# Optimization experiments

Measured on AMD Instinct MI355X. Metric: run time of the kernel, lower is better.

Reference implementation:

```python
import jax, jax.numpy as jnp
import numpy as np

NUM_HEADS = 16
THETA = 10000.0


def setup_inputs() -> dict:
    key = jax.random.key(0)
    ks = jax.random.split(key, 5)
    B, S, D = 2, 2048, 1024
    scale = 1.0 / np.sqrt(D)
    return {
        "x": jax.random.normal(ks[0], (B, S, D), dtype=jnp.float32),
        "Wq": jax.random.normal(ks[1], (D, D), dtype=jnp.float32) * scale,
        "Wk": jax.random.normal(ks[2], (D, D), dtype=jnp.float32) * scale,
        "Wv": jax.random.normal(ks[3], (D, D), dtype=jnp.float32) * scale,
        "Wo": jax.random.normal(ks[4], (D, D), dtype=jnp.float32) * scale,
    }


def _rope(t, cos, sin):
    # t: [B, H, S, d_k], interleaved pair rotation.
    t1 = t[..., 0::2]
    t2 = t[..., 1::2]
    r1 = t1 * cos - t2 * sin
    r2 = t1 * sin + t2 * cos
    # re-interleave
    out = jnp.stack([r1, r2], axis=-1)
    return out.reshape(t.shape)


def reference(x, Wq, Wk, Wv, Wo):
    B, S, D = x.shape
    H = NUM_HEADS
    dk = D // H

    # projections (Linear: y = x @ W^T)
    Q = jnp.einsum("bsd,ed->bse", x, Wq).reshape(B, S, H, dk).transpose(0, 2, 1, 3)
    K = jnp.einsum("bsd,ed->bse", x, Wk).reshape(B, S, H, dk).transpose(0, 2, 1, 3)
    V = jnp.einsum("bsd,ed->bse", x, Wv).reshape(B, S, H, dk).transpose(0, 2, 1, 3)

    # RoPE angles: [S, dk/2]
    inv_freq = THETA ** (-jnp.arange(0, dk, 2, dtype=jnp.float32) / dk)
    ang = jnp.arange(S, dtype=jnp.float32)[:, None] * inv_freq[None, :]
    cos, sin = jnp.cos(ang), jnp.sin(ang)  # broadcast over [B, H, S, dk/2]
    Q = _rope(Q, cos, sin)
    K = _rope(K, cos, sin)

    # causal SDPA
    scores = jnp.einsum("bhqd,bhkd->bhqk", Q, K) / jnp.sqrt(jnp.float32(dk))
    causal = jnp.tril(jnp.ones((S, S), dtype=bool))
    scores = jnp.where(causal, scores, jnp.finfo(scores.dtype).min)
    attn = jax.nn.softmax(scores, axis=-1)
    out = jnp.einsum("bhqk,bhkd->bhqd", attn, V)

    out = out.transpose(0, 2, 1, 3).reshape(B, S, D)
    return jnp.einsum("bsd,ed->bse", out, Wo)
```

## Files before the change

### kernel.cpp

```cpp
#include <hip/hip_runtime.h>
#include <hip/hip_bf16.h>

#define B_   2
#define S_   2048
#define H_   16
#define DK_  64
#define D_   1024
#define BS_  4096
#define N3_  3072

typedef __attribute__((ext_vector_type(8))) short short8;
typedef __attribute__((ext_vector_type(4))) float floatx4;
typedef __hip_bfloat16 bf16;

__device__ inline void load_lds16(const bf16* g, bf16* l) {
    __builtin_amdgcn_global_load_lds(
        (const __attribute__((address_space(1))) void*)g,
        (__attribute__((address_space(3))) void*)l, 16, 0, 0);
}

__device__ inline unsigned int pack2bf16(float a, float b) {
    __hip_bfloat162 h = __float22bfloat162_rn(make_float2(a, b));
    return *(unsigned int*)&h;
}

__global__ void cvt_all(const float* __restrict__ x,  const float* __restrict__ wq,
                        const float* __restrict__ wk, const float* __restrict__ wv,
                        const float* __restrict__ wo,
                        bf16* __restrict__ xb, bf16* __restrict__ wcat, bf16* __restrict__ wob) {
    const int blk = blockIdx.x;
    const float* src; bf16* dst; int base;
    if (blk < 4096)      { src = x;  dst = xb;             base = blk * 1024; }
    else if (blk < 5120) { src = wq; dst = wcat;           base = (blk - 4096) * 1024; }
    else if (blk < 6144) { src = wk; dst = wcat + 1048576; base = (blk - 5120) * 1024; }
    else if (blk < 7168) { src = wv; dst = wcat + 2097152; base = (blk - 6144) * 1024; }
    else                 { src = wo; dst = wob;            base = (blk - 7168) * 1024; }
    const int i = base + threadIdx.x * 4;
    float4 v = *(const float4*)(src + i);
    *(uint2*)(dst + i) = make_uint2(pack2bf16(v.x, v.y), pack2bf16(v.z, v.w));
}

__global__ __launch_bounds__(256)
void gemm_qkv(const bf16* __restrict__ A, const bf16* __restrict__ Bw,
              bf16* __restrict__ Cqk, bf16* __restrict__ Vt) {
    __shared__ __align__(16) bf16 lA[128 * 32];
    __shared__ __align__(16) bf16 lB[128 * 32];
    const int t = threadIdx.x;
    const int lane = t & 63, w = t >> 6;
    const int quad = lane >> 4, l16 = lane & 15;
    const int m0 = blockIdx.x * 128, n0 = blockIdx.y * 128;
    const int wm = (w & 1) * 64, wn = (w >> 1) * 64;

    floatx4 acc[4][4];
#pragma unroll
    for (int i = 0; i < 4; i++)
#pragma unroll
        for (int j = 0; j < 4; j++) acc[i][j] = (floatx4){0.f, 0.f, 0.f, 0.f};

    const int srow = t >> 2;
    const int scol = (t & 3) * 8;
    const bf16* pA0 = A + (size_t)(m0 + srow) * D_ + scol;
    const bf16* pA1 = A + (size_t)(m0 + 64 + srow) * D_ + scol;
    const bf16* pB0 = Bw + (size_t)(n0 + srow) * D_ + scol;
    const bf16* pB1 = Bw + (size_t)(n0 + 64 + srow) * D_ + scol;

    for (int kt = 0; kt < D_; kt += 32) {
        load_lds16(pA0, lA + t * 8);
        load_lds16(pA1, lA + 2048 + t * 8);
        load_lds16(pB0, lB + t * 8);
        load_lds16(pB1, lB + 2048 + t * 8);
        pA0 += 32; pA1 += 32; pB0 += 32; pB1 += 32;
        __syncthreads();

        short8 af[4], bfr[4];
#pragma unroll
        for (int i = 0; i < 4; i++)
            af[i] = *(const short8*)&lA[(wm + i * 16 + l16) * 32 + quad * 8];
#pragma unroll
        for (int j = 0; j < 4; j++)
            bfr[j] = *(const short8*)&lB[(wn + j * 16 + l16) * 32 + quad * 8];
#pragma unroll
        for (int i = 0; i < 4; i++)
#pragma unroll
            for (int j = 0; j < 4; j++)
                acc[i][j] = __builtin_amdgcn_mfma_f32_16x16x32_bf16(af[i], bfr[j], acc[i][j], 0, 0, 0);
        __syncthreads();
    }

    if (n0 < 2 * D_) {
#pragma unroll
        for (int i = 0; i < 4; i++) {
            const int row = m0 + wm + i * 16 + quad * 4;
#pragma unroll
            for (int j = 0; j < 4; j++) {
                const int col = n0 + wn + j * 16 + l16;
#pragma unroll
                for (int r = 0; r < 4; r++)
                    Cqk[(size_t)(row + r) * N3_ + col] = __float2bfloat16(acc[i][j][r]);
            }
        }
    } else {
#pragma unroll
        for (int i = 0; i < 4; i++) {
            const int row0 = m0 + wm + i * 16 + quad * 4;
            const int bb = row0 >> 11;
            const int ss = row0 & 2047;
#pragma unroll
            for (int j = 0; j < 4; j++) {
                const int c = n0 + wn + j * 16 + l16 - 2 * D_;
                const int h = c >> 6, d = c & 63;
                *(uint2*)(Vt + (((size_t)bb * H_ + h) * 64 + d) * S_ + ss) =
                    make_uint2(pack2bf16(acc[i][j][0], acc[i][j][1]),
                               pack2bf16(acc[i][j][2], acc[i][j][3]));
            }
        }
    }
}

__global__ void rope_kernel(const bf16* __restrict__ QKV,
                            bf16* __restrict__ Qr, bf16* __restrict__ Kr) {
    int tid = blockIdx.x * blockDim.x + threadIdx.x;
    if (tid >= B_ * S_ * H_ * 32) return;
    const int i = tid & 31;
    const int h = (tid >> 5) & (H_ - 1);
    const int bs = tid >> 9;
    const int s = bs & (S_ - 1);
    const int b = bs >> 11;

    const bf16* base = QKV + (size_t)bs * N3_ + h * 64 + 2 * i;
    const float q0 = __bfloat162float(base[0]);
    const float q1 = __bfloat162float(base[1]);
    const float k0 = __bfloat162float(base[D_]);
    const float k1 = __bfloat162float(base[D_ + 1]);

    const float freq = exp2f(-(float)(2 * i) * 0.2076205059304601f);
    const float ang = (float)s * freq;
    float sn, cs;
    sincosf(ang, &sn, &cs);

    const float QS = 0.18033688011112042f;
    const size_t off = ((size_t)(b * H_ + h) * S_ + s) * 64 + 2 * i;
    *(unsigned int*)(Qr + off) = pack2bf16((q0 * cs - q1 * sn) * QS, (q0 * sn + q1 * cs) * QS);
    *(unsigned int*)(Kr + off) = pack2bf16(k0 * cs - k1 * sn, k0 * sn + k1 * cs);
}

__global__ __launch_bounds__(256)
void attn_kernel(const bf16* __restrict__ Qr, const bf16* __restrict__ Kr,
                 const bf16* __restrict__ Vt, bf16* __restrict__ Ob) {
    __shared__ __align__(16) bf16 lK0[64 * 64], lK1[64 * 64];
    __shared__ __align__(16) bf16 lV0[64 * 64], lV1[64 * 64];
    __shared__ __align__(16) bf16 lP[4][16][36];

    const int t = threadIdx.x;
    const int w = t >> 6, lane = t & 63;
    const int quad = lane >> 4, l16 = lane & 15;
    const int bh = blockIdx.y;
    const int b = bh >> 4, h = bh & 15;
    const int qblk = 31 - (int)blockIdx.x;
    const int q0w = qblk * 64 + w * 16;
    const int q = q0w + l16;

    const bf16* Qb = Qr + (size_t)bh * S_ * 64;
    const bf16* Kb = Kr + (size_t)bh * S_ * 64;
    const bf16* Vb = Vt + (size_t)bh * 64 * S_;

    const int srow = t >> 3;
    const int sj   = (t & 7) ^ (srow & 7);
    const int swz = l16 & 7;
    const int pA = quad ^ swz;
    const int pB = (4 + quad) ^ swz;

    const bf16* qrow = Qb + (size_t)q * 64;
    short8 bq[2];
    bq[0] = *(const short8*)(qrow + quad * 8);
    bq[1] = *(const short8*)(qrow + 32 + quad * 8);

    float lacc = 0.f;
    floatx4 o[4];
#pragma unroll
    for (int ct = 0; ct < 4; ct++) o[ct] = (floatx4){0.f, 0.f, 0.f, 0.f};

    auto stage = [&](bf16* dK, bf16* dV, int kb) {
        const bf16* gK = Kb + (size_t)(kb + srow) * 64 + sj * 8;
        const bf16* gV = Vb + (size_t)srow * S_ + kb + sj * 8;
        load_lds16(gK,                   dK + t * 8);
        load_lds16(gK + 32 * 64,         dK + 2048 + t * 8);
        load_lds16(gV,                   dV + t * 8);
        load_lds16(gV + (size_t)32 * S_, dV + 2048 + t * 8);
    };

    auto computeStep = [&](const bf16* lKc, const bf16* lVc, int kb, bool need_mask) {
#pragma unroll
        for (int c = 0; c < 2; c++) {
            floatx4 s[2];
#pragma unroll
            for (int k2 = 0; k2 < 2; k2++) {
                const int kt = c * 2 + k2;
                const short8 k0 = *(const short8*)&lKc[(kt * 16 + l16) * 64 + pA * 8];
                const short8 k1 = *(const short8*)&lKc[(kt * 16 + l16) * 64 + pB * 8];
                floatx4 z = (floatx4){0.f, 0.f, 0.f, 0.f};
                z = __builtin_amdgcn_mfma_f32_16x16x32_bf16(k0, bq[0], z, 0, 0, 0);
                z = __builtin_amdgcn_mfma_f32_16x16x32_bf16(k1, bq[1], z, 0, 0, 0);
                s[k2] = z;
            }
            float rs = 0.f;
#pragma unroll
            for (int k2 = 0; k2 < 2; k2++) {
                float p[4];
#pragma unroll
                for (int r = 0; r < 4; r++) {
                    float v = s[k2][r];
                    if (need_mask) {
                        const int key = kb + (c * 2 + k2) * 16 + quad * 4 + r;
                        if (key > q) v = -1e30f;
                    }
                    p[r] = __builtin_amdgcn_exp2f(v);
                    rs += p[r];
                }
                *(uint2*)&lP[w][l16][k2 * 16 + quad * 4] =
                    make_uint2(pack2bf16(p[0], p[1]), pack2bf16(p[2], p[3]));
            }
            lacc += rs;
            const int pc = c ? pB : pA;
            const short8 bp = *(const short8*)&lP[w][l16][quad * 8];
#pragma unroll
            for (int ct = 0; ct < 4; ct++) {
                const short8 av = *(const short8*)&lVc[(ct * 16 + l16) * 64 + pc * 8];
                o[ct] = __builtin_amdgcn_mfma_f32_16x16x32_bf16(av, bp, o[ct], 0, 0, 0);
            }
        }
    };

    const int nsteps = qblk + 1;
    stage(lK0, lV0, 0);
    __syncthreads();
    for (int st = 0; st < nsteps; ++st) {
        const bool even = (st & 1) == 0;
        const bf16* cK = even ? lK0 : lK1;  const bf16* cV = even ? lV0 : lV1;
        bf16* nK = even ? lK1 : lK0;        bf16* nV = even ? lV1 : lV0;
        if (st + 1 < nsteps) stage(nK, nV, (st + 1) * 64);
        computeStep(cK, cV, st * 64, st == nsteps - 1);
        __syncthreads();
    }

    float l = lacc;
    l += __shfl_xor(l, 16);
    l += __shfl_xor(l, 32);
    const float invl = 1.0f / l;
    bf16* orow = Ob + ((size_t)(b * S_ + q) * H_ + h) * 64;
#pragma unroll
    for (int ct = 0; ct < 4; ct++)
        *(uint2*)(orow + ct * 16 + quad * 4) =
            make_uint2(pack2bf16(o[ct][0] * invl, o[ct][1] * invl),
                       pack2bf16(o[ct][2] * invl, o[ct][3] * invl));
}

__global__ __launch_bounds__(256)
void gemm_out(const bf16* __restrict__ A, const bf16* __restrict__ Bw,
              float* __restrict__ C) {
    __shared__ __align__(16) bf16 lA[128 * 32];
    __shared__ __align__(16) bf16 lB[64 * 32];
    const int t = threadIdx.x;
    const int lane = t & 63, w = t >> 6;
    const int quad = lane >> 4, l16 = lane & 15;
    const int m0 = blockIdx.x * 128, n0 = blockIdx.y * 64;
    const int wm = (w & 1) * 64, wn = (w >> 1) * 32;

    floatx4 acc[4][2];
#pragma unroll
    for (int i = 0; i < 4; i++)
#pragma unroll
        for (int j = 0; j < 2; j++) acc[i][j] = (floatx4){0.f, 0.f, 0.f, 0.f};

    const int srow = t >> 2;
    const int scol = (t & 3) * 8;
    const bf16* pA0 = A + (size_t)(m0 + srow) * D_ + scol;
    const bf16* pA1 = A + (size_t)(m0 + 64 + srow) * D_ + scol;
    const bf16* pB0 = Bw + (size_t)(n0 + srow) * D_ + scol;

    for (int kt = 0; kt < D_; kt += 32) {
        load_lds16(pA0, lA + t * 8);
        load_lds16(pA1, lA + 2048 + t * 8);
        load_lds16(pB0, lB + t * 8);
        pA0 += 32; pA1 += 32; pB0 += 32;
        __syncthreads();

        short8 af[4], bfr[2];
#pragma unroll
        for (int i = 0; i < 4; i++)
            af[i] = *(const short8*)&lA[(wm + i * 16 + l16) * 32 + quad * 8];
#pragma unroll
        for (int j = 0; j < 2; j++)
            bfr[j] = *(const short8*)&lB[(wn + j * 16 + l16) * 32 + quad * 8];
#pragma unroll
        for (int i = 0; i < 4; i++)
#pragma unroll
            for (int j = 0; j < 2; j++)
                acc[i][j] = __builtin_amdgcn_mfma_f32_16x16x32_bf16(af[i], bfr[j], acc[i][j], 0, 0, 0);
        __syncthreads();
    }

#pragma unroll
    for (int i = 0; i < 4; i++) {
        const int row = m0 + wm + i * 16 + quad * 4;
#pragma unroll
        for (int j = 0; j < 2; j++) {
            const int col = n0 + wn + j * 16 + l16;
#pragma unroll
            for (int r = 0; r < 4; r++)
                C[(size_t)(row + r) * D_ + col] = acc[i][j][r];
        }
    }
}

extern "C" void kernel_launch(void* const* d_in, const int* in_sizes, int n_in,
                              void* d_out, int out_size, void* d_ws, size_t ws_size,
                              hipStream_t stream) {
    const float* x  = (const float*)d_in[0];
    const float* Wq = (const float*)d_in[1];
    const float* Wk = (const float*)d_in[2];
    const float* Wv = (const float*)d_in[3];
    const float* Wo = (const float*)d_in[4];
    float* out = (float*)d_out;

    char* ws = (char*)d_ws;
    bf16* xb   = (bf16*)(ws);
    bf16* Wcat = (bf16*)(ws + 8388608);
    bf16* Wob  = (bf16*)(ws + 14680064);
    bf16* QKVb = (bf16*)(ws + 16777216);
    bf16* Qr   = (bf16*)(ws + 41943040);
    bf16* Kr   = (bf16*)(ws + 50331648);
    bf16* Vt   = (bf16*)(ws + 58720256);
    bf16* Ob   = QKVb;

    cvt_all<<<8192, 256, 0, stream>>>(x, Wq, Wk, Wv, Wo, xb, Wcat, Wob);
    gemm_qkv<<<dim3(32, 24), 256, 0, stream>>>(xb, Wcat, QKVb, Vt);
    rope_kernel<<<8192, 256, 0, stream>>>(QKVb, Qr, Kr);
    attn_kernel<<<dim3(32, B_ * H_), 256, 0, stream>>>(Qr, Kr, Vt, Ob);
    gemm_out<<<dim3(32, 16), 256, 0, stream>>>(Ob, Wob, out);
}
```

Measured before the change: 203.7 us.

## Use 32x32 MFMA in attention and K=64 swizzled LDS tiles in GEMMs

The attention kernel drops to 128 threads, with two waves of 32 query rows each. Both QK^T and PV now use the 32x32x16 bf16 MFMA, with a swizzled K/V LDS layout and a reshaped P staging buffer. Both GEMMs double the K tile to 64 per iteration and XOR-swizzle the LDS layout, which halves the barrier count and should avoid bank conflicts. The costs are more registers in attention, fewer waves per block, and larger LDS use in the GEMMs.

```diff
diff --git a/kernel.cpp b/kernel.cpp
--- a/kernel.cpp
+++ b/kernel.cpp
@@ -11,6 +11,7 @@
 
 typedef __attribute__((ext_vector_type(8))) short short8;
 typedef __attribute__((ext_vector_type(4))) float floatx4;
+typedef __attribute__((ext_vector_type(16))) float floatx16;
 typedef __hip_bfloat16 bf16;
 
 __device__ inline void load_lds16(const bf16* g, bf16* l) {
@@ -43,8 +44,8 @@
 __global__ __launch_bounds__(256)
 void gemm_qkv(const bf16* __restrict__ A, const bf16* __restrict__ Bw,
               bf16* __restrict__ Cqk, bf16* __restrict__ Vt) {
-    __shared__ __align__(16) bf16 lA[128 * 32];
-    __shared__ __align__(16) bf16 lB[128 * 32];
+    __shared__ __align__(16) bf16 lA[128 * 64];
+    __shared__ __align__(16) bf16 lB[128 * 64];
     const int t = threadIdx.x;
     const int lane = t & 63, w = t >> 6;
     const int quad = lane >> 4, l16 = lane & 15;
@@ -57,33 +58,39 @@
 #pragma unroll
         for (int j = 0; j < 4; j++) acc[i][j] = (floatx4){0.f, 0.f, 0.f, 0.f};
 
-    const int srow = t >> 2;
-    const int scol = (t & 3) * 8;
-    const bf16* pA0 = A + (size_t)(m0 + srow) * D_ + scol;
-    const bf16* pA1 = A + (size_t)(m0 + 64 + srow) * D_ + scol;
-    const bf16* pB0 = Bw + (size_t)(n0 + srow) * D_ + scol;
-    const bf16* pB1 = Bw + (size_t)(n0 + 64 + srow) * D_ + scol;
-
-    for (int kt = 0; kt < D_; kt += 32) {
-        load_lds16(pA0, lA + t * 8);
-        load_lds16(pA1, lA + 2048 + t * 8);
-        load_lds16(pB0, lB + t * 8);
-        load_lds16(pB1, lB + 2048 + t * 8);
-        pA0 += 32; pA1 += 32; pB0 += 32; pB1 += 32;
-        __syncthreads();
-
-        short8 af[4], bfr[4];
-#pragma unroll
-        for (int i = 0; i < 4; i++)
-            af[i] = *(const short8*)&lA[(wm + i * 16 + l16) * 32 + quad * 8];
-#pragma unroll
-        for (int j = 0; j < 4; j++)
-            bfr[j] = *(const short8*)&lB[(wn + j * 16 + l16) * 32 + quad * 8];
-#pragma unroll
-        for (int i = 0; i < 4; i++)
-#pragma unroll
-            for (int j = 0; j < 4; j++)
-                acc[i][j] = __builtin_amdgcn_mfma_f32_16x16x32_bf16(af[i], bfr[j], acc[i][j], 0, 0, 0);
+    const int srow = t >> 3;
+    const int sj   = (t & 7) ^ (srow & 7);
+
+    for (int kt = 0; kt < D_; kt += 64) {
+#pragma unroll
+        for (int r = 0; r < 4; r++)
+            load_lds16(A + (size_t)(m0 + r * 32 + srow) * D_ + kt + sj * 8,
+                       lA + r * 2048 + t * 8);
+#pragma unroll
+        for (int r = 0; r < 4; r++)
+            load_lds16(Bw + (size_t)(n0 + r * 32 + srow) * D_ + kt + sj * 8,
+                       lB + r * 2048 + t * 8);
+        __syncthreads();
+
+#pragma unroll
+        for (int kh = 0; kh < 2; kh++) {
+            short8 af[4], bfr[4];
+#pragma unroll
+            for (int i = 0; i < 4; i++) {
+                const int row = wm + i * 16 + l16;
+                af[i] = *(const short8*)&lA[row * 64 + ((kh * 4 + quad) ^ (row & 7)) * 8];
+            }
+#pragma unroll
+            for (int j = 0; j < 4; j++) {
+                const int row = wn + j * 16 + l16;
+                bfr[j] = *(const short8*)&lB[row * 64 + ((kh * 4 + quad) ^ (row & 7)) * 8];
+            }
+#pragma unroll
+            for (int i = 0; i < 4; i++)
+#pragma unroll
+                for (int j = 0; j < 4; j++)
+                    acc[i][j] = __builtin_amdgcn_mfma_f32_16x16x32_bf16(af[i], bfr[j], acc[i][j], 0, 0, 0);
+        }
         __syncthreads();
     }
 
@@ -144,21 +151,20 @@
     *(unsigned int*)(Kr + off) = pack2bf16(k0 * cs - k1 * sn, k0 * sn + k1 * cs);
 }
 
-__global__ __launch_bounds__(256)
+__global__ __launch_bounds__(128)
 void attn_kernel(const bf16* __restrict__ Qr, const bf16* __restrict__ Kr,
                  const bf16* __restrict__ Vt, bf16* __restrict__ Ob) {
     __shared__ __align__(16) bf16 lK0[64 * 64], lK1[64 * 64];
     __shared__ __align__(16) bf16 lV0[64 * 64], lV1[64 * 64];
-    __shared__ __align__(16) bf16 lP[4][16][36];
+    __shared__ __align__(16) bf16 lP[2][32][34];
 
     const int t = threadIdx.x;
     const int w = t >> 6, lane = t & 63;
-    const int quad = lane >> 4, l16 = lane & 15;
+    const int l32 = lane & 31, hi = lane >> 5;
     const int bh = blockIdx.y;
     const int b = bh >> 4, h = bh & 15;
     const int qblk = 31 - (int)blockIdx.x;
-    const int q0w = qblk * 64 + w * 16;
-    const int q = q0w + l16;
+    const int q = qblk * 64 + w * 32 + l32;
 
     const bf16* Qb = Qr + (size_t)bh * S_ * 64;
     const bf16* Kb = Kr + (size_t)bh * S_ * 64;
@@ -166,67 +172,72 @@
 
     const int srow = t >> 3;
     const int sj   = (t & 7) ^ (srow & 7);
-    const int swz = l16 & 7;
-    const int pA = quad ^ swz;
-    const int pB = (4 + quad) ^ swz;
-
-    const bf16* qrow = Qb + (size_t)q * 64;
-    short8 bq[2];
-    bq[0] = *(const short8*)(qrow + quad * 8);
-    bq[1] = *(const short8*)(qrow + 32 + quad * 8);
+
+    short8 bq[4];
+    {
+        const bf16* qrow = Qb + (size_t)q * 64;
+#pragma unroll
+        for (int ks = 0; ks < 4; ks++)
+            bq[ks] = *(const short8*)(qrow + ks * 16 + hi * 8);
+    }
 
     float lacc = 0.f;
-    floatx4 o[4];
-#pragma unroll
-    for (int ct = 0; ct < 4; ct++) o[ct] = (floatx4){0.f, 0.f, 0.f, 0.f};
+    floatx16 o[2];
+#pragma unroll
+    for (int dt = 0; dt < 2; dt++)
+#pragma unroll
+        for (int r = 0; r < 16; r++) o[dt][r] = 0.f;
 
     auto stage = [&](bf16* dK, bf16* dV, int kb) {
-        const bf16* gK = Kb + (size_t)(kb + srow) * 64 + sj * 8;
-        const bf16* gV = Vb + (size_t)srow * S_ + kb + sj * 8;
-        load_lds16(gK,                   dK + t * 8);
-        load_lds16(gK + 32 * 64,         dK + 2048 + t * 8);
-        load_lds16(gV,                   dV + t * 8);
-        load_lds16(gV + (size_t)32 * S_, dV + 2048 + t * 8);
+#pragma unroll
+        for (int r = 0; r < 4; r++)
+            load_lds16(Kb + (size_t)(kb + r * 16 + srow) * 64 + sj * 8,
+                       dK + r * 1024 + t * 8);
+#pragma unroll
+        for (int r = 0; r < 4; r++)
+            load_lds16(Vb + (size_t)(r * 16 + srow) * S_ + kb + sj * 8,
+                       dV + r * 1024 + t * 8);
     };
 
     auto computeStep = [&](const bf16* lKc, const bf16* lVc, int kb, bool need_mask) {
 #pragma unroll
-        for (int c = 0; c < 2; c++) {
-            floatx4 s[2];
-#pragma unroll
-            for (int k2 = 0; k2 < 2; k2++) {
-                const int kt = c * 2 + k2;
-                const short8 k0 = *(const short8*)&lKc[(kt * 16 + l16) * 64 + pA * 8];
-                const short8 k1 = *(const short8*)&lKc[(kt * 16 + l16) * 64 + pB * 8];
-                floatx4 z = (floatx4){0.f, 0.f, 0.f, 0.f};
-                z = __builtin_amdgcn_mfma_f32_16x16x32_bf16(k0, bq[0], z, 0, 0, 0);
-                z = __builtin_amdgcn_mfma_f32_16x16x32_bf16(k1, bq[1], z, 0, 0, 0);
-                s[k2] = z;
-            }
-            float rs = 0.f;
-#pragma unroll
-            for (int k2 = 0; k2 < 2; k2++) {
-                float p[4];
-#pragma unroll
-                for (int r = 0; r < 4; r++) {
-                    float v = s[k2][r];
-                    if (need_mask) {
-                        const int key = kb + (c * 2 + k2) * 16 + quad * 4 + r;
-                        if (key > q) v = -1e30f;
-                    }
-                    p[r] = __builtin_amdgcn_exp2f(v);
-                    rs += p[r];
+        for (int kt = 0; kt < 2; kt++) {
+            floatx16 z;
+#pragma unroll
+            for (int r = 0; r < 16; r++) z[r] = 0.f;
+            const int krow = kt * 32 + l32;
+#pragma unroll
+            for (int ks = 0; ks < 4; ks++) {
+                const short8 ak = *(const short8*)
+                    &lKc[krow * 64 + (((ks * 2 + hi) ^ (krow & 7)) * 8)];
+                z = __builtin_amdgcn_mfma_f32_32x32x16_bf16(ak, bq[ks], z, 0, 0, 0);
+            }
+            float p[16];
+#pragma unroll
+            for (int r = 0; r < 16; r++) {
+                float v = z[r];
+                if (need_mask) {
+                    const int key = kb + kt * 32 + (r & 3) + 8 * (r >> 2) + 4 * hi;
+                    if (key > q) v = -1e30f;
                 }
-                *(uint2*)&lP[w][l16][k2 * 16 + quad * 4] =
-                    make_uint2(pack2bf16(p[0], p[1]), pack2bf16(p[2], p[3]));
-            }
-            lacc += rs;
-            const int pc = c ? pB : pA;
-            const short8 bp = *(const short8*)&lP[w][l16][quad * 8];
-#pragma unroll
-            for (int ct = 0; ct < 4; ct++) {
-                const short8 av = *(const short8*)&lVc[(ct * 16 + l16) * 64 + pc * 8];
-                o[ct] = __builtin_amdgcn_mfma_f32_16x16x32_bf16(av, bp, o[ct], 0, 0, 0);
+                p[r] = __builtin_amdgcn_exp2f(v);
+                lacc += p[r];
+            }
+#pragma unroll
+            for (int rq = 0; rq < 4; rq++)
+                *(uint2*)&lP[w][l32][8 * rq + 4 * hi] =
+                    make_uint2(pack2bf16(p[rq * 4 + 0], p[rq * 4 + 1]),
+                               pack2bf16(p[rq * 4 + 2], p[rq * 4 + 3]));
+#pragma unroll
+            for (int kl = 0; kl < 2; kl++) {
+                const short8 bp = *(const short8*)&lP[w][l32][kl * 16 + hi * 8];
+#pragma unroll
+                for (int dt = 0; dt < 2; dt++) {
+                    const int vrow = dt * 32 + l32;
+                    const short8 av = *(const short8*)
+                        &lVc[vrow * 64 + (((kt * 4 + kl * 2 + hi) ^ (vrow & 7)) * 8)];
+                    o[dt] = __builtin_amdgcn_mfma_f32_32x32x16_bf16(av, bp, o[dt], 0, 0, 0);
+                }
             }
         }
     };
@@ -243,23 +254,25 @@
         __syncthreads();
     }
 
-    float l = lacc;
-    l += __shfl_xor(l, 16);
-    l += __shfl_xor(l, 32);
+    float l = lacc + __shfl_xor(lacc, 32);
     const float invl = 1.0f / l;
     bf16* orow = Ob + ((size_t)(b * S_ + q) * H_ + h) * 64;
 #pragma unroll
-    for (int ct = 0; ct < 4; ct++)
-        *(uint2*)(orow + ct * 16 + quad * 4) =
-            make_uint2(pack2bf16(o[ct][0] * invl, o[ct][1] * invl),
-                       pack2bf16(o[ct][2] * invl, o[ct][3] * invl));
+    for (int dt = 0; dt < 2; dt++)
+#pragma unroll
+        for (int rq = 0; rq < 4; rq++) {
+            const int d = dt * 32 + 8 * rq + 4 * hi;
+            *(uint2*)(orow + d) =
+                make_uint2(pack2bf16(o[dt][rq * 4 + 0] * invl, o[dt][rq * 4 + 1] * invl),
+                           pack2bf16(o[dt][rq * 4 + 2] * invl, o[dt][rq * 4 + 3] * invl));
+        }
 }
 
 __global__ __launch_bounds__(256)
 void gemm_out(const bf16* __restrict__ A, const bf16* __restrict__ Bw,
               float* __restrict__ C) {
-    __shared__ __align__(16) bf16 lA[128 * 32];
-    __shared__ __align__(16) bf16 lB[64 * 32];
+    __shared__ __align__(16) bf16 lA[128 * 64];
+    __shared__ __align__(16) bf16 lB[64 * 64];
     const int t = threadIdx.x;
     const int lane = t & 63, w = t >> 6;
     const int quad = lane >> 4, l16 = lane & 15;
@@ -272,31 +285,39 @@
 #pragma unroll
         for (int j = 0; j < 2; j++) acc[i][j] = (floatx4){0.f, 0.f, 0.f, 0.f};
 
-    const int srow = t >> 2;
-    const int scol = (t & 3) * 8;
-    const bf16* pA0 = A + (size_t)(m0 + srow) * D_ + scol;
-    const bf16* pA1 = A + (size_t)(m0 + 64 + srow) * D_ + scol;
-    const bf16* pB0 = Bw + (size_t)(n0 + srow) * D_ + scol;
-
-    for (int kt = 0; kt < D_; kt += 32) {
-        load_lds16(pA0, lA + t * 8);
-        load_lds16(pA1, lA + 2048 + t * 8);
-        load_lds16(pB0, lB + t * 8);
-        pA0 += 32; pA1 += 32; pB0 += 32;
-        __syncthreads();
-
-        short8 af[4], bfr[2];
-#pragma unroll
-        for (int i = 0; i < 4; i++)
-            af[i] = *(const short8*)&lA[(wm + i * 16 + l16) * 32 + quad * 8];
-#pragma unroll
-        for (int j = 0; j < 2; j++)
-            bfr[j] = *(const short8*)&lB[(wn + j * 16 + l16) * 32 + quad * 8];
-#pragma unroll
-        for (int i = 0; i < 4; i++)
-#pragma unroll
-            for (int j = 0; j < 2; j++)
-                acc[i][j] = __builtin_amdgcn_mfma_f32_16x16x32_bf16(af[i], bfr[j], acc[i][j], 0, 0, 0);
+    const int srow = t >> 3;
+    const int sj   = (t & 7) ^ (srow & 7);
+
+    for (int kt = 0; kt < D_; kt += 64) {
+#pragma unroll
+        for (int r = 0; r < 4; r++)
+            load_lds16(A + (size_t)(m0 + r * 32 + srow) * D_ + kt + sj * 8,
+                       lA + r * 2048 + t * 8);
+#pragma unroll
+        for (int r = 0; r < 2; r++)
+            load_lds16(Bw + (size_t)(n0 + r * 32 + srow) * D_ + kt + sj * 8,
+                       lB + r * 2048 + t * 8);
+        __syncthreads();
+
+#pragma unroll
+        for (int kh = 0; kh < 2; kh++) {
+            short8 af[4], bfr[2];
+#pragma unroll
+            for (int i = 0; i < 4; i++) {
+                const int row = wm + i * 16 + l16;
+                af[i] = *(const short8*)&lA[row * 64 + ((kh * 4 + quad) ^ (row & 7)) * 8];
+            }
+#pragma unroll
+            for (int j = 0; j < 2; j++) {
+                const int row = wn + j * 16 + l16;
+                bfr[j] = *(const short8*)&lB[row * 64 + ((kh * 4 + quad) ^ (row & 7)) * 8];
+            }
+#pragma unroll
+            for (int i = 0; i < 4; i++)
+#pragma unroll
+                for (int j = 0; j < 2; j++)
+                    acc[i][j] = __builtin_amdgcn_mfma_f32_16x16x32_bf16(af[i], bfr[j], acc[i][j], 0, 0, 0);
+        }
         __syncthreads();
     }
 
@@ -336,6 +357,6 @@
     cvt_all<<<8192, 256, 0, stream>>>(x, Wq, Wk, Wv, Wo, xb, Wcat, Wob);
     gemm_qkv<<<dim3(32, 24), 256, 0, stream>>>(xb, Wcat, QKVb, Vt);
     rope_kernel<<<8192, 256, 0, stream>>>(QKVb, Qr, Kr);
-    attn_kernel<<<dim3(32, B_ * H_), 256, 0, stream>>>(Qr, Kr, Vt, Ob);
+    attn_kernel<<<dim3(32, B_ * H_), 128, 0, stream>>>(Qr, Kr, Vt, Ob);
     gemm_out<<<dim3(32, 16), 256, 0, stream>>>(Ob, Wob, out);
 }
```

New measurement: 208.9 us. 2.5% more time.

## Deepen GEMM K-tiles with swizzled LDS and use 128-query attention blocks

Applied to the files above, without the earlier changes.

Both projection GEMMs now stage 64-wide K slices per barrier pair instead of 32, with an XOR swizzle on the LDS layout. This halves the number of synchronisations and is meant to reduce LDS bank conflicts. The attention kernel runs 512 threads over 128 query rows, so each staged K/V tile serves twice as many queries. Each wave skips compute past its own causal limit but still joins the shared staging, which adds some imbalance across waves and more register pressure.

```diff
diff --git a/kernel.cpp b/kernel.cpp
--- a/kernel.cpp
+++ b/kernel.cpp
@@ -43,8 +43,8 @@
 __global__ __launch_bounds__(256)
 void gemm_qkv(const bf16* __restrict__ A, const bf16* __restrict__ Bw,
               bf16* __restrict__ Cqk, bf16* __restrict__ Vt) {
-    __shared__ __align__(16) bf16 lA[128 * 32];
-    __shared__ __align__(16) bf16 lB[128 * 32];
+    __shared__ __align__(16) bf16 lA[128 * 64];
+    __shared__ __align__(16) bf16 lB[128 * 64];
     const int t = threadIdx.x;
     const int lane = t & 63, w = t >> 6;
     const int quad = lane >> 4, l16 = lane & 15;
@@ -57,33 +57,39 @@
 #pragma unroll
         for (int j = 0; j < 4; j++) acc[i][j] = (floatx4){0.f, 0.f, 0.f, 0.f};
 
-    const int srow = t >> 2;
-    const int scol = (t & 3) * 8;
-    const bf16* pA0 = A + (size_t)(m0 + srow) * D_ + scol;
-    const bf16* pA1 = A + (size_t)(m0 + 64 + srow) * D_ + scol;
-    const bf16* pB0 = Bw + (size_t)(n0 + srow) * D_ + scol;
-    const bf16* pB1 = Bw + (size_t)(n0 + 64 + srow) * D_ + scol;
-
-    for (int kt = 0; kt < D_; kt += 32) {
-        load_lds16(pA0, lA + t * 8);
-        load_lds16(pA1, lA + 2048 + t * 8);
-        load_lds16(pB0, lB + t * 8);
-        load_lds16(pB1, lB + 2048 + t * 8);
-        pA0 += 32; pA1 += 32; pB0 += 32; pB1 += 32;
-        __syncthreads();
-
-        short8 af[4], bfr[4];
-#pragma unroll
-        for (int i = 0; i < 4; i++)
-            af[i] = *(const short8*)&lA[(wm + i * 16 + l16) * 32 + quad * 8];
-#pragma unroll
-        for (int j = 0; j < 4; j++)
-            bfr[j] = *(const short8*)&lB[(wn + j * 16 + l16) * 32 + quad * 8];
-#pragma unroll
-        for (int i = 0; i < 4; i++)
-#pragma unroll
-            for (int j = 0; j < 4; j++)
-                acc[i][j] = __builtin_amdgcn_mfma_f32_16x16x32_bf16(af[i], bfr[j], acc[i][j], 0, 0, 0);
+    const int srow = t >> 3;
+    const int sj   = (t & 7) ^ (srow & 7);
+
+    for (int kt = 0; kt < D_; kt += 64) {
+#pragma unroll
+        for (int r = 0; r < 4; r++)
+            load_lds16(A + (size_t)(m0 + r * 32 + srow) * D_ + kt + sj * 8,
+                       lA + r * 2048 + t * 8);
+#pragma unroll
+        for (int r = 0; r < 4; r++)
+            load_lds16(Bw + (size_t)(n0 + r * 32 + srow) * D_ + kt + sj * 8,
+                       lB + r * 2048 + t * 8);
+        __syncthreads();
+
+#pragma unroll
+        for (int kh = 0; kh < 2; kh++) {
+            short8 af[4], bfr[4];
+#pragma unroll
+            for (int i = 0; i < 4; i++) {
+                const int row = wm + i * 16 + l16;
+                af[i] = *(const short8*)&lA[row * 64 + ((kh * 4 + quad) ^ (row & 7)) * 8];
+            }
+#pragma unroll
+            for (int j = 0; j < 4; j++) {
+                const int row = wn + j * 16 + l16;
+                bfr[j] = *(const short8*)&lB[row * 64 + ((kh * 4 + quad) ^ (row & 7)) * 8];
+            }
+#pragma unroll
+            for (int i = 0; i < 4; i++)
+#pragma unroll
+                for (int j = 0; j < 4; j++)
+                    acc[i][j] = __builtin_amdgcn_mfma_f32_16x16x32_bf16(af[i], bfr[j], acc[i][j], 0, 0, 0);
+        }
         __syncthreads();
     }
 
@@ -144,20 +150,20 @@
     *(unsigned int*)(Kr + off) = pack2bf16(k0 * cs - k1 * sn, k0 * sn + k1 * cs);
 }
 
-__global__ __launch_bounds__(256)
+__global__ __launch_bounds__(512)
 void attn_kernel(const bf16* __restrict__ Qr, const bf16* __restrict__ Kr,
                  const bf16* __restrict__ Vt, bf16* __restrict__ Ob) {
     __shared__ __align__(16) bf16 lK0[64 * 64], lK1[64 * 64];
     __shared__ __align__(16) bf16 lV0[64 * 64], lV1[64 * 64];
-    __shared__ __align__(16) bf16 lP[4][16][36];
+    __shared__ __align__(16) bf16 lP[8][16][36];
 
     const int t = threadIdx.x;
     const int w = t >> 6, lane = t & 63;
     const int quad = lane >> 4, l16 = lane & 15;
     const int bh = blockIdx.y;
     const int b = bh >> 4, h = bh & 15;
-    const int qblk = 31 - (int)blockIdx.x;
-    const int q0w = qblk * 64 + w * 16;
+    const int qblk = 15 - (int)blockIdx.x;
+    const int q0w = qblk * 128 + w * 16;
     const int q = q0w + l16;
 
     const bf16* Qb = Qr + (size_t)bh * S_ * 64;
@@ -181,12 +187,8 @@
     for (int ct = 0; ct < 4; ct++) o[ct] = (floatx4){0.f, 0.f, 0.f, 0.f};
 
     auto stage = [&](bf16* dK, bf16* dV, int kb) {
-        const bf16* gK = Kb + (size_t)(kb + srow) * 64 + sj * 8;
-        const bf16* gV = Vb + (size_t)srow * S_ + kb + sj * 8;
-        load_lds16(gK,                   dK + t * 8);
-        load_lds16(gK + 32 * 64,         dK + 2048 + t * 8);
-        load_lds16(gV,                   dV + t * 8);
-        load_lds16(gV + (size_t)32 * S_, dV + 2048 + t * 8);
+        load_lds16(Kb + (size_t)(kb + srow) * 64 + sj * 8, dK + t * 8);
+        load_lds16(Vb + (size_t)srow * S_ + kb + sj * 8,   dV + t * 8);
     };
 
     auto computeStep = [&](const bf16* lKc, const bf16* lVc, int kb, bool need_mask) {
@@ -231,7 +233,8 @@
         }
     };
 
-    const int nsteps = qblk + 1;
+    const int nsteps = 2 * qblk + 2;
+    const int nst_w  = (q0w + 79) >> 6;
     stage(lK0, lV0, 0);
     __syncthreads();
     for (int st = 0; st < nsteps; ++st) {
@@ -239,7 +242,7 @@
         const bf16* cK = even ? lK0 : lK1;  const bf16* cV = even ? lV0 : lV1;
         bf16* nK = even ? lK1 : lK0;        bf16* nV = even ? lV1 : lV0;
         if (st + 1 < nsteps) stage(nK, nV, (st + 1) * 64);
-        computeStep(cK, cV, st * 64, st == nsteps - 1);
+        if (st < nst_w) computeStep(cK, cV, st * 64, st == nst_w - 1);
         __syncthreads();
     }
 
@@ -258,8 +261,8 @@
 __global__ __launch_bounds__(256)
 void gemm_out(const bf16* __restrict__ A, const bf16* __restrict__ Bw,
               float* __restrict__ C) {
-    __shared__ __align__(16) bf16 lA[128 * 32];
-    __shared__ __align__(16) bf16 lB[64 * 32];
+    __shared__ __align__(16) bf16 lA[128 * 64];
+    __shared__ __align__(16) bf16 lB[64 * 64];
     const int t = threadIdx.x;
     const int lane = t & 63, w = t >> 6;
     const int quad = lane >> 4, l16 = lane & 15;
@@ -272,31 +275,39 @@
 #pragma unroll
         for (int j = 0; j < 2; j++) acc[i][j] = (floatx4){0.f, 0.f, 0.f, 0.f};
 
-    const int srow = t >> 2;
-    const int scol = (t & 3) * 8;
-    const bf16* pA0 = A + (size_t)(m0 + srow) * D_ + scol;
-    const bf16* pA1 = A + (size_t)(m0 + 64 + srow) * D_ + scol;
-    const bf16* pB0 = Bw + (size_t)(n0 + srow) * D_ + scol;
-
-    for (int kt = 0; kt < D_; kt += 32) {
-        load_lds16(pA0, lA + t * 8);
-        load_lds16(pA1, lA + 2048 + t * 8);
-        load_lds16(pB0, lB + t * 8);
-        pA0 += 32; pA1 += 32; pB0 += 32;
-        __syncthreads();
-
-        short8 af[4], bfr[2];
-#pragma unroll
-        for (int i = 0; i < 4; i++)
-            af[i] = *(const short8*)&lA[(wm + i * 16 + l16) * 32 + quad * 8];
-#pragma unroll
-        for (int j = 0; j < 2; j++)
-            bfr[j] = *(const short8*)&lB[(wn + j * 16 + l16) * 32 + quad * 8];
-#pragma unroll
-        for (int i = 0; i < 4; i++)
-#pragma unroll
-            for (int j = 0; j < 2; j++)
-                acc[i][j] = __builtin_amdgcn_mfma_f32_16x16x32_bf16(af[i], bfr[j], acc[i][j], 0, 0, 0);
+    const int srow = t >> 3;
+    const int sj   = (t & 7) ^ (srow & 7);
+
+    for (int kt = 0; kt < D_; kt += 64) {
+#pragma unroll
+        for (int r = 0; r < 4; r++)
+            load_lds16(A + (size_t)(m0 + r * 32 + srow) * D_ + kt + sj * 8,
+                       lA + r * 2048 + t * 8);
+#pragma unroll
+        for (int r = 0; r < 2; r++)
+            load_lds16(Bw + (size_t)(n0 + r * 32 + srow) * D_ + kt + sj * 8,
+                       lB + r * 2048 + t * 8);
+        __syncthreads();
+
+#pragma unroll
+        for (int kh = 0; kh < 2; kh++) {
+            short8 af[4], bfr[2];
+#pragma unroll
+            for (int i = 0; i < 4; i++) {
+                const int row = wm + i * 16 + l16;
+                af[i] = *(const short8*)&lA[row * 64 + ((kh * 4 + quad) ^ (row & 7)) * 8];
+            }
+#pragma unroll
+            for (int j = 0; j < 2; j++) {
+                const int row = wn + j * 16 + l16;
+                bfr[j] = *(const short8*)&lB[row * 64 + ((kh * 4 + quad) ^ (row & 7)) * 8];
+            }
+#pragma unroll
+            for (int i = 0; i < 4; i++)
+#pragma unroll
+                for (int j = 0; j < 2; j++)
+                    acc[i][j] = __builtin_amdgcn_mfma_f32_16x16x32_bf16(af[i], bfr[j], acc[i][j], 0, 0, 0);
+        }
         __syncthreads();
     }
 
@@ -336,6 +347,6 @@
     cvt_all<<<8192, 256, 0, stream>>>(x, Wq, Wk, Wv, Wo, xb, Wcat, Wob);
     gemm_qkv<<<dim3(32, 24), 256, 0, stream>>>(xb, Wcat, QKVb, Vt);
     rope_kernel<<<8192, 256, 0, stream>>>(QKVb, Qr, Kr);
-    attn_kernel<<<dim3(32, B_ * H_), 256, 0, stream>>>(Qr, Kr, Vt, Ob);
+    attn_kernel<<<dim3(16, B_ * H_), 512, 0, stream>>>(Qr, Kr, Vt, Ob);
     gemm_out<<<dim3(32, 16), 256, 0, stream>>>(Ob, Wob, out);
 }
```

Result: faster. 197.1 us (-3.3%).
